# Optimization experiments

Measured on AMD Instinct MI355X. Metric: run time of the kernel, lower is better.

## Reference

```python
import jax, jax.numpy as jnp
import numpy as np

EPS = 1e-4

def _softmax_kernel(data, projection_matrix, is_query):
    # data: [..., n, d], projection_matrix: [m, d]
    d = data.shape[-1]
    m = projection_matrix.shape[0]
    data_normalizer = 1.0 / (d ** 0.25)
    ratio = 1.0 / (m ** 0.5)
    # [..., n, m]
    data_dash = jnp.einsum('...id,jd->...ij', data_normalizer * data, projection_matrix)
    # ||x||^2 / 2 * normalizer^2, shape [..., n, 1]
    diag_data = (jnp.sum(data * data, axis=-1) * 0.5 * data_normalizer ** 2)[..., None]
    if is_query:
        stab = jnp.max(data_dash, axis=-1, keepdims=True)
    else:
        stab = jnp.max(data_dash)
    return ratio * (jnp.exp(data_dash - diag_data - stab) + EPS)

def _linear_attention(q, k, v):
    # q,k: [..., n, m] feature maps; v: [..., n, e]
    D_inv = 1.0 / jnp.einsum('...nd,...d->...n', q, k.sum(axis=-2))
    context = jnp.einsum('...nd,...ne->...de', k, v)  # [..., m, e]
    return jnp.einsum('...de,...nd,...n->...ne', context, q, D_inv)

def setup_inputs() -> dict:
    key = jax.random.key(0)
    k1, k2, k3, k4 = jax.random.split(key, 4)
    B, H, N, D, M = 8, 8, 4096, 64, 266
    return {
        'q': jax.random.normal(k1, (B, H, N, D), dtype=jnp.float32),
        'k': jax.random.normal(k2, (B, H, N, D), dtype=jnp.float32),
        'v': jax.random.normal(k3, (B, H, N, D), dtype=jnp.float32),
        'projection_matrix': jax.random.normal(k4, (M, D), dtype=jnp.float32),
    }

def reference(q, k, v, projection_matrix):
    q_prime = _softmax_kernel(q, projection_matrix, is_query=True)
    k_prime = _softmax_kernel(k, projection_matrix, is_query=False)
    return _linear_attention(q_prime, k_prime, v)
```

## Files before the change

### kernel.cpp

```cpp
#include <hip/hip_runtime.h>
#include <math.h>

#define BH    64
#define NSEQ  4096
#define DDIM  64
#define MDIM  266
#define MPAD  272
#define KTS   40
#define RATIO 0.06131393394849658f
#define NORMF 0.35355339059327373f
#define DIAGF 0.0625f
#define EPSF  1e-4f

typedef __attribute__((ext_vector_type(8))) short bf16x8;
typedef __attribute__((ext_vector_type(4))) float f32x4;

__device__ __forceinline__ unsigned fenc(float f) {
  unsigned u = __float_as_uint(f);
  return (u & 0x80000000u) ? ~u : (u | 0x80000000u);
}
__device__ __forceinline__ float fdec(unsigned u) {
  return (u & 0x80000000u) ? __uint_as_float(u & 0x7fffffffu) : __uint_as_float(~u);
}

__device__ __forceinline__ void split1(float x, unsigned short& h, unsigned short& l) {
  unsigned ux = __float_as_uint(x);
  float hf = __uint_as_float(ux & 0xffff0000u);
  h = (unsigned short)(ux >> 16);
  l = (unsigned short)(__float_as_uint(x - hf) >> 16);
}

__device__ __forceinline__ void splitf(float4 a, float4 b, bf16x8& hi, bf16x8& lo) {
  float x[8] = {a.x, a.y, a.z, a.w, b.x, b.y, b.z, b.w};
#pragma unroll
  for (int e = 0; e < 8; ++e) {
    unsigned short h, l;
    split1(x[e], h, l);
    hi[e] = (short)h;
    lo[e] = (short)l;
  }
}

__device__ __forceinline__ f32x4 mfma3(bf16x8 ah, bf16x8 al, bf16x8 bh, bf16x8 bl, f32x4 acc) {
  acc = __builtin_amdgcn_mfma_f32_16x16x32_bf16(ah, bh, acc, 0, 0, 0);
  acc = __builtin_amdgcn_mfma_f32_16x16x32_bf16(ah, bl, acc, 0, 0, 0);
  acc = __builtin_amdgcn_mfma_f32_16x16x32_bf16(al, bh, acc, 0, 0, 0);
  return acc;
}

__global__ __launch_bounds__(256) void pprep_kernel(const float* __restrict__ proj,
                                                    short* __restrict__ phi,
                                                    short* __restrict__ plo) {
  int idx = blockIdx.x * 256 + threadIdx.x;
  if (idx >= MPAD * DDIM) return;
  int j = idx >> 6;
  float x = (j < MDIM) ? proj[idx] : 0.f;
  unsigned short h, l;
  split1(x, h, l);
  phi[idx] = (short)h;
  plo[idx] = (short)l;
}

__global__ __launch_bounds__(256) void kmax_kernel(const float* __restrict__ k,
                                                   const short* __restrict__ phi,
                                                   const short* __restrict__ plo,
                                                   unsigned* __restrict__ kmax) {
  __shared__ float sK[64 * 76];
  __shared__ float wmax[4];
  const int tid = threadIdx.x;
  const int lane = tid & 63, wv = tid >> 6, lrow = lane & 15, lgrp = lane >> 4;

  float tmax = -1e30f;
  for (int it = 0; it < 8; ++it) {
    const int chunk = blockIdx.x * 8 + it;
    const int bh = chunk >> 6, ch = chunk & 63;
    const float* kb = k + ((size_t)bh * NSEQ + (size_t)ch * 64) * DDIM;
    __syncthreads();
#pragma unroll
    for (int t = 0; t < 4; ++t) {
      int fid = tid + t * 256, r = fid >> 4, d4 = fid & 15;
      *(float4*)&sK[r * 76 + d4 * 4] = ((const float4*)kb)[fid];
    }
    __syncthreads();

    bf16x8 ahi[2], alo[2];
#pragma unroll
    for (int s = 0; s < 2; ++s) {
      const float* p = &sK[(wv * 16 + lrow) * 76 + s * 32 + lgrp * 8];
      splitf(*(const float4*)p, *(const float4*)(p + 4), ahi[s], alo[s]);
    }

#pragma unroll
    for (int jt = 0; jt < 17; ++jt) {
      f32x4 acc = {0.f, 0.f, 0.f, 0.f};
#pragma unroll
      for (int s = 0; s < 2; ++s) {
        const size_t bo = ((size_t)(jt * 16 + lrow)) * DDIM + s * 32 + lgrp * 8;
        acc = mfma3(ahi[s], alo[s], *(const bf16x8*)(phi + bo), *(const bf16x8*)(plo + bo), acc);
      }
      if (jt < 16 || lrow < 10) {
#pragma unroll
        for (int i = 0; i < 4; ++i) tmax = fmaxf(tmax, acc[i]);
      }
    }
  }
#pragma unroll
  for (int off = 32; off; off >>= 1) tmax = fmaxf(tmax, __shfl_xor(tmax, off));
  if (lane == 0) wmax[wv] = tmax;
  __syncthreads();
  if (tid == 0) {
    float m = fmaxf(fmaxf(wmax[0], wmax[1]), fmaxf(wmax[2], wmax[3]));
    atomicMax(kmax, fenc(m * NORMF));
  }
}

__device__ __forceinline__ float dash_reg(int jt, const bf16x8* ahi, const bf16x8* alo,
                                          const bf16x8* ph, const bf16x8* pl,
                                          const float* sDiag, float stab,
                                          unsigned short* kThi, unsigned short* kTlo,
                                          int lrow, int lgrp) {
  float kssum = 0.f;
  const int jg = jt * 16 + lrow;
#pragma unroll
  for (int m = 0; m < 2; ++m) {
    f32x4 d = {0.f, 0.f, 0.f, 0.f};
#pragma unroll
    for (int s = 0; s < 2; ++s)
      d = mfma3(ahi[m * 2 + s], alo[m * 2 + s], ph[s], pl[s], d);
    ushort4 h4, l4;
#pragma unroll
    for (int i = 0; i < 4; ++i) {
      const int nl = m * 16 + lgrp * 4 + i;
      float kd = d[i] * NORMF;
      float kp = (jg < MDIM) ? RATIO * (__expf(kd - sDiag[nl] - stab) + EPSF) : 0.f;
      kssum += kp;
      unsigned short h, l;
      split1(kp, h, l);
      ((unsigned short*)&h4)[i] = h;
      ((unsigned short*)&l4)[i] = l;
    }
    *(ushort4*)&kThi[(size_t)jg * KTS + m * 16 + lgrp * 4] = h4;
    *(ushort4*)&kTlo[(size_t)jg * KTS + m * 16 + lgrp * 4] = l4;
  }
  return kssum;
}

__global__ __launch_bounds__(256, 2) void ctx_kernel(const float* __restrict__ k,
                                                     const float* __restrict__ v,
                                                     const short* __restrict__ phi,
                                                     const short* __restrict__ plo,
                                                     const unsigned* __restrict__ kmaxp,
                                                     float* __restrict__ ctxp,
                                                     float* __restrict__ ksump) {
  __shared__ unsigned short kThi[MPAD * KTS];
  __shared__ unsigned short kTlo[MPAD * KTS];
  __shared__ float sV[32 * 68];
  __shared__ float sDiag[32];
  float* sK = (float*)kThi;

  const int tid = threadIdx.x;
  const int lane = tid & 63, wv = tid >> 6, lrow = lane & 15, lgrp = lane >> 4;
  const int bh = blockIdx.x & 63, c8 = blockIdx.x >> 6;
  const float stab = fdec(*kmaxp);
  const float* kb = k + ((size_t)bh * NSEQ + (size_t)c8 * 512) * DDIM;
  const float* vb = v + ((size_t)bh * NSEQ + (size_t)c8 * 512) * DDIM;

  bf16x8 pfh[4][2], pfl[4][2];
#pragma unroll
  for (int t = 0; t < 4; ++t)
#pragma unroll
    for (int s = 0; s < 2; ++s) {
      const size_t bo = ((size_t)((t * 4 + wv) * 16 + lrow)) * DDIM + s * 32 + lgrp * 8;
      pfh[t][s] = *(const bf16x8*)(phi + bo);
      pfl[t][s] = *(const bf16x8*)(plo + bo);
    }
  bf16x8 pfh4[2], pfl4[2];
  if (wv == 0) {
#pragma unroll
    for (int s = 0; s < 2; ++s) {
      const size_t bo = ((size_t)(256 + lrow)) * DDIM + s * 32 + lgrp * 8;
      pfh4[s] = *(const bf16x8*)(phi + bo);
      pfl4[s] = *(const bf16x8*)(plo + bo);
    }
  }

  f32x4 acc[17];
#pragma unroll
  for (int jt = 0; jt < 17; ++jt) acc[jt] = (f32x4){0.f, 0.f, 0.f, 0.f};
  float ks[5] = {0.f, 0.f, 0.f, 0.f, 0.f};

  for (int rt = 0; rt < 16; ++rt) {
#pragma unroll
    for (int t = 0; t < 2; ++t) {
      int fid = tid + t * 256, r = fid >> 4, d4 = fid & 15;
      *(float4*)&sK[r * 76 + d4 * 4] = ((const float4*)(kb + (size_t)rt * 32 * DDIM))[fid];
      *(float4*)&sV[r * 68 + d4 * 4] = ((const float4*)(vb + (size_t)rt * 32 * DDIM))[fid];
    }
    __syncthreads();
    if (tid < 32) {
      float s = 0.f;
      const float* row = &sK[tid * 76];
#pragma unroll
      for (int d = 0; d < 64; d += 4) {
        float4 x = *(const float4*)(row + d);
        s = fmaf(x.x, x.x, fmaf(x.y, x.y, fmaf(x.z, x.z, fmaf(x.w, x.w, s))));
      }
      sDiag[tid] = s * DIAGF;
    }
    bf16x8 ahi[4], alo[4];
#pragma unroll
    for (int m = 0; m < 2; ++m)
#pragma unroll
      for (int s = 0; s < 2; ++s) {
        const float* p = &sK[(m * 16 + lrow) * 76 + s * 32 + lgrp * 8];
        splitf(*(const float4*)p, *(const float4*)(p + 4), ahi[m * 2 + s], alo[m * 2 + s]);
      }
    bf16x8 vbh, vbl;
    {
      float tv[8];
#pragma unroll
      for (int q = 0; q < 8; ++q) tv[q] = sV[(lgrp * 8 + q) * 68 + wv * 16 + lrow];
      splitf(make_float4(tv[0], tv[1], tv[2], tv[3]),
             make_float4(tv[4], tv[5], tv[6], tv[7]), vbh, vbl);
    }
    __syncthreads();

#pragma unroll
    for (int t = 0; t < 4; ++t)
      ks[t] += dash_reg(t * 4 + wv, ahi, alo, pfh[t], pfl[t], sDiag, stab,
                        kThi, kTlo, lrow, lgrp);
    if (wv == 0)
      ks[4] += dash_reg(16, ahi, alo, pfh4, pfl4, sDiag, stab, kThi, kTlo, lrow, lgrp);
    __syncthreads();

#pragma unroll
    for (int jt = 0; jt < 17; ++jt) {
      bf16x8 ah = *(const bf16x8*)&kThi[(size_t)(jt * 16 + lrow) * KTS + lgrp * 8];
      bf16x8 al = *(const bf16x8*)&kTlo[(size_t)(jt * 16 + lrow) * KTS + lgrp * 8];
      acc[jt] = mfma3(ah, al, vbh, vbl, acc[jt]);
    }
    __syncthreads();
  }

  float* ksb = ksump + (size_t)(c8 * BH + bh) * MPAD;
#pragma unroll
  for (int t = 0; t < 4; ++t) {
    float s = ks[t];
    s += __shfl_xor(s, 16);
    s += __shfl_xor(s, 32);
    if (lgrp == 0) ksb[(t * 4 + wv) * 16 + lrow] = s;
  }
  if (wv == 0) {
    float s = ks[4];
    s += __shfl_xor(s, 16);
    s += __shfl_xor(s, 32);
    if (lgrp == 0) ksb[256 + lrow] = s;
  }
  float* cxb = ctxp + (size_t)(c8 * BH + bh) * MPAD * DDIM;
#pragma unroll
  for (int jt = 0; jt < 17; ++jt)
#pragma unroll
    for (int i = 0; i < 4; ++i)
      cxb[(size_t)(jt * 16 + lgrp * 4 + i) * DDIM + wv * 16 + lrow] = acc[jt][i];
}

__global__ __launch_bounds__(256) void reduce_kernel(const float* __restrict__ ctxp,
                                                     const float* __restrict__ ksump,
                                                     float* __restrict__ ctx,
                                                     float* __restrict__ ksum) {
  const size_t SL = (size_t)BH * MPAD * DDIM;
  const int gid = blockIdx.x * 256 + threadIdx.x;
  if (gid < (int)(SL / 4)) {
    float4 s = make_float4(0.f, 0.f, 0.f, 0.f);
#pragma unroll
    for (int c = 0; c < 8; ++c) {
      float4 x = ((const float4*)ctxp)[c * (SL / 4) + gid];
      s.x += x.x; s.y += x.y; s.z += x.z; s.w += x.w;
    }
    ((float4*)ctx)[gid] = s;
  }
  if (gid < BH * MPAD) {
    float s = 0.f;
#pragma unroll
    for (int c = 0; c < 8; ++c) s += ksump[(size_t)c * BH * MPAD + gid];
    ksum[gid] = s;
  }
}

__global__ __launch_bounds__(256, 2) void out_kernel(const float* __restrict__ q,
                                                     const short* __restrict__ phi,
                                                     const short* __restrict__ plo,
                                                     const float* __restrict__ ctx,
                                                     const float* __restrict__ ksum,
                                                     float* __restrict__ out) {
  __shared__ float buf[64 * 76];
  __shared__ float sCtx[64 * 68];
  __shared__ float sDiag[64];
  __shared__ float sKs[MPAD];
  unsigned short* qThi = (unsigned short*)buf;
  unsigned short* qTlo = qThi + 64 * 72;
  const int tid = threadIdx.x;
  const int lane = tid & 63, wv = tid >> 6, lrow = lane & 15, lgrp = lane >> 4;
  const int bh = blockIdx.x & 63, rc = blockIdx.x >> 6;
  const float* qb = q + ((size_t)bh * NSEQ + (size_t)rc * 64) * DDIM;

#pragma unroll
  for (int t = 0; t < 4; ++t) {
    int fid = tid + t * 256, r = fid >> 4, d4 = fid & 15;
    *(float4*)&buf[r * 76 + d4 * 4] = ((const float4*)qb)[fid];
  }
  for (int t = tid; t < MPAD; t += 256) sKs[t] = (t < MDIM) ? ksum[(size_t)bh * MPAD + t] : 0.f;
  __syncthreads();
  if (tid < 64) {
    float s = 0.f;
    const float* row = &buf[tid * 76];
#pragma unroll
    for (int d = 0; d < 64; d += 4) {
      float4 x = *(const float4*)(row + d);
      s = fmaf(x.x, x.x, fmaf(x.y, x.y, fmaf(x.z, x.z, fmaf(x.w, x.w, s))));
    }
    sDiag[tid] = s * DIAGF;
  }
  bf16x8 ahi[2], alo[2];
#pragma unroll
  for (int s = 0; s < 2; ++s) {
    const float* p = &buf[(wv * 16 + lrow) * 76 + s * 32 + lgrp * 8];
    splitf(*(const float4*)p, *(const float4*)(p + 4), ahi[s], alo[s]);
  }
  __syncthreads();

  f32x4 qd[17];
#pragma unroll
  for (int jt = 0; jt < 17; ++jt) {
    f32x4 a = {0.f, 0.f, 0.f, 0.f};
#pragma unroll
    for (int s = 0; s < 2; ++s) {
      const size_t bo = ((size_t)(jt * 16 + lrow)) * DDIM + s * 32 + lgrp * 8;
      a = mfma3(ahi[s], alo[s], *(const bf16x8*)(phi + bo), *(const bf16x8*)(plo + bo), a);
    }
#pragma unroll
    for (int i = 0; i < 4; ++i) qd[jt][i] = a[i] * NORMF;
  }

  float di[4];
#pragma unroll
  for (int i = 0; i < 4; ++i) {
    float m = -1e30f;
#pragma unroll
    for (int jt = 0; jt < 17; ++jt)
      if (jt < 16 || lrow < 10) m = fmaxf(m, qd[jt][i]);
    m = fmaxf(m, __shfl_xor(m, 1));
    m = fmaxf(m, __shfl_xor(m, 2));
    m = fmaxf(m, __shfl_xor(m, 4));
    m = fmaxf(m, __shfl_xor(m, 8));
    const float dg = sDiag[wv * 16 + lgrp * 4 + i];
    float s = 0.f;
#pragma unroll
    for (int jt = 0; jt < 17; ++jt) {
      const int jg = jt * 16 + lrow;
      float val = (jg < MDIM) ? RATIO * (__expf(qd[jt][i] - dg - m) + EPSF) : 0.f;
      qd[jt][i] = val;
      s = fmaf(val, sKs[jg], s);
    }
    s += __shfl_xor(s, 1);
    s += __shfl_xor(s, 2);
    s += __shfl_xor(s, 4);
    s += __shfl_xor(s, 8);
    di[i] = 1.0f / s;
  }

  f32x4 accO[4];
#pragma unroll
  for (int mt = 0; mt < 4; ++mt) accO[mt] = (f32x4){0.f, 0.f, 0.f, 0.f};

#pragma unroll
  for (int c = 0; c < 5; ++c) {
    const int nwr = (c < 4) ? 4 : 2;
    const int nks = (c < 4) ? 2 : 1;
    const int jn = (c < 4) ? 64 : 10;
#pragma unroll
    for (int t = 0; t < nwr; ++t) {
      const int jt = c * 4 + t;
#pragma unroll
      for (int i = 0; i < 4; ++i) {
        unsigned short h = 0, l = 0;
        if (jt < 17) split1(qd[jt][i] * di[i], h, l);
        qThi[(wv * 16 + lgrp * 4 + i) * 72 + t * 16 + lrow] = h;
        qTlo[(wv * 16 + lgrp * 4 + i) * 72 + t * 16 + lrow] = l;
      }
    }
#pragma unroll
    for (int t = 0; t < 4; ++t) {
      int fid = tid + t * 256, r = fid >> 4, e4 = fid & 15;
      if (r < jn)
        *(float4*)&sCtx[r * 68 + e4 * 4] =
            ((const float4*)(ctx + ((size_t)bh * MPAD + c * 64 + r) * DDIM))[e4];
    }
    __syncthreads();
#pragma unroll
    for (int ks2 = 0; ks2 < nks; ++ks2) {
      float tv[8];
#pragma unroll
      for (int e = 0; e < 8; ++e)
        tv[e] = sCtx[(ks2 * 32 + lgrp * 8 + e) * 68 + wv * 16 + lrow];
      bf16x8 cbh, cbl;
      splitf(make_float4(tv[0], tv[1], tv[2], tv[3]),
             make_float4(tv[4], tv[5], tv[6], tv[7]), cbh, cbl);
#pragma unroll
      for (int mt = 0; mt < 4; ++mt) {
        bf16x8 ah = *(const bf16x8*)&qThi[(mt * 16 + lrow) * 72 + ks2 * 32 + lgrp * 8];
        bf16x8 al = *(const bf16x8*)&qTlo[(mt * 16 + lrow) * 72 + ks2 * 32 + lgrp * 8];
        accO[mt] = mfma3(ah, al, cbh, cbl, accO[mt]);
      }
    }
    __syncthreads();
  }

#pragma unroll
  for (int mt = 0; mt < 4; ++mt) {
#pragma unroll
    for (int i = 0; i < 4; ++i) {
      const int r = mt * 16 + lgrp * 4 + i;
      out[((size_t)bh * NSEQ + (size_t)rc * 64 + r) * DDIM + wv * 16 + lrow] = accO[mt][i];
    }
  }
}

extern "C" void kernel_launch(void* const* d_in, const int* in_sizes, int n_in,
                              void* d_out, int out_size, void* d_ws, size_t ws_size,
                              hipStream_t stream) {
  (void)in_sizes; (void)n_in; (void)out_size; (void)ws_size;
  const float* q = (const float*)d_in[0];
  const float* k = (const float*)d_in[1];
  const float* v = (const float*)d_in[2];
  const float* proj = (const float*)d_in[3];
  float* out = (float*)d_out;

  unsigned* kmax = (unsigned*)d_ws;
  float* ctx = (float*)((char*)d_ws + 256);
  float* ksum = ctx + (size_t)BH * MPAD * DDIM;
  short* phi = (short*)(ksum + (size_t)BH * MPAD);
  short* plo = phi + (size_t)MPAD * DDIM;

  const size_t SL = (size_t)BH * MPAD * DDIM;
  float* ctxp = (float*)d_out;
  float* ksump = ctxp + 8 * SL;

  hipMemsetAsync(d_ws, 0, 256, stream);
  pprep_kernel<<<dim3((MPAD * DDIM + 255) / 256), dim3(256), 0, stream>>>(proj, phi, plo);
  kmax_kernel<<<dim3(512), dim3(256), 0, stream>>>(k, phi, plo, kmax);
  ctx_kernel<<<dim3(BH * 8), dim3(256), 0, stream>>>(k, v, phi, plo, kmax, ctxp, ksump);
  reduce_kernel<<<dim3((unsigned)(SL / 4 / 256)), dim3(256), 0, stream>>>(ctxp, ksump, ctx, ksum);
  out_kernel<<<dim3(BH * 64), dim3(256), 0, stream>>>(q, phi, plo, ctx, ksum, out);
}
```

Measured before the change: 325.2 us.

## Make out_kernel persistent per 512 rows, holding split ctx in registers

The output kernel now launches 512 blocks instead of 4096. Each block loops over 16 tiles of 32 query rows and loads the context matrix once, split into bf16 hi/lo register fragments, reusing it for every tile instead of restaging it in shared memory per 64-row block. The projection work is now divided across the four waves by feature column instead of by row. This needs cross-wave max and sum reductions through shared memory plus extra barriers per tile. Fewer blocks and heavy register use (9 hi/lo fragment pairs) may lower occupancy and latency hiding on the 256-CU device.

```diff
diff --git a/kernel.cpp b/kernel.cpp
--- a/kernel.cpp
+++ b/kernel.cpp
@@ -7,6 +7,7 @@
 #define MDIM  266
 #define MPAD  272
 #define KTS   40
+#define QTS   296
 #define RATIO 0.06131393394849658f
 #define NORMF 0.35355339059327373f
 #define DIAGF 0.0625f
@@ -293,135 +294,215 @@
                                                      const float* __restrict__ ctx,
                                                      const float* __restrict__ ksum,
                                                      float* __restrict__ out) {
-  __shared__ float buf[64 * 76];
-  __shared__ float sCtx[64 * 68];
-  __shared__ float sDiag[64];
+  __shared__ unsigned short qThi[32 * QTS];
+  __shared__ unsigned short qTlo[32 * QTS];
+  __shared__ float sQ[32 * 76];
   __shared__ float sKs[MPAD];
-  unsigned short* qThi = (unsigned short*)buf;
-  unsigned short* qTlo = qThi + 64 * 72;
+  __shared__ float sDiag[32];
+  __shared__ float sMax[4 * 32];
+  __shared__ float sSum[4 * 32];
   const int tid = threadIdx.x;
   const int lane = tid & 63, wv = tid >> 6, lrow = lane & 15, lgrp = lane >> 4;
-  const int bh = blockIdx.x & 63, rc = blockIdx.x >> 6;
-  const float* qb = q + ((size_t)bh * NSEQ + (size_t)rc * 64) * DDIM;
-
-#pragma unroll
-  for (int t = 0; t < 4; ++t) {
-    int fid = tid + t * 256, r = fid >> 4, d4 = fid & 15;
-    *(float4*)&buf[r * 76 + d4 * 4] = ((const float4*)qb)[fid];
-  }
-  for (int t = tid; t < MPAD; t += 256) sKs[t] = (t < MDIM) ? ksum[(size_t)bh * MPAD + t] : 0.f;
-  __syncthreads();
-  if (tid < 64) {
-    float s = 0.f;
-    const float* row = &buf[tid * 76];
-#pragma unroll
-    for (int d = 0; d < 64; d += 4) {
-      float4 x = *(const float4*)(row + d);
-      s = fmaf(x.x, x.x, fmaf(x.y, x.y, fmaf(x.z, x.z, fmaf(x.w, x.w, s))));
-    }
-    sDiag[tid] = s * DIAGF;
-  }
-  bf16x8 ahi[2], alo[2];
-#pragma unroll
-  for (int s = 0; s < 2; ++s) {
-    const float* p = &buf[(wv * 16 + lrow) * 76 + s * 32 + lgrp * 8];
-    splitf(*(const float4*)p, *(const float4*)(p + 4), ahi[s], alo[s]);
-  }
-  __syncthreads();
-
-  f32x4 qd[17];
-#pragma unroll
-  for (int jt = 0; jt < 17; ++jt) {
-    f32x4 a = {0.f, 0.f, 0.f, 0.f};
-#pragma unroll
-    for (int s = 0; s < 2; ++s) {
-      const size_t bo = ((size_t)(jt * 16 + lrow)) * DDIM + s * 32 + lgrp * 8;
-      a = mfma3(ahi[s], alo[s], *(const bf16x8*)(phi + bo), *(const bf16x8*)(plo + bo), a);
-    }
-#pragma unroll
-    for (int i = 0; i < 4; ++i) qd[jt][i] = a[i] * NORMF;
-  }
-
-  float di[4];
-#pragma unroll
-  for (int i = 0; i < 4; ++i) {
-    float m = -1e30f;
-#pragma unroll
-    for (int jt = 0; jt < 17; ++jt)
-      if (jt < 16 || lrow < 10) m = fmaxf(m, qd[jt][i]);
-    m = fmaxf(m, __shfl_xor(m, 1));
-    m = fmaxf(m, __shfl_xor(m, 2));
-    m = fmaxf(m, __shfl_xor(m, 4));
-    m = fmaxf(m, __shfl_xor(m, 8));
-    const float dg = sDiag[wv * 16 + lgrp * 4 + i];
-    float s = 0.f;
-#pragma unroll
-    for (int jt = 0; jt < 17; ++jt) {
-      const int jg = jt * 16 + lrow;
-      float val = (jg < MDIM) ? RATIO * (__expf(qd[jt][i] - dg - m) + EPSF) : 0.f;
-      qd[jt][i] = val;
-      s = fmaf(val, sKs[jg], s);
-    }
-    s += __shfl_xor(s, 1);
-    s += __shfl_xor(s, 2);
-    s += __shfl_xor(s, 4);
-    s += __shfl_xor(s, 8);
-    di[i] = 1.0f / s;
-  }
-
-  f32x4 accO[4];
-#pragma unroll
-  for (int mt = 0; mt < 4; ++mt) accO[mt] = (f32x4){0.f, 0.f, 0.f, 0.f};
-
-#pragma unroll
-  for (int c = 0; c < 5; ++c) {
-    const int nwr = (c < 4) ? 4 : 2;
-    const int nks = (c < 4) ? 2 : 1;
-    const int jn = (c < 4) ? 64 : 10;
-#pragma unroll
-    for (int t = 0; t < nwr; ++t) {
-      const int jt = c * 4 + t;
+  const int bh = blockIdx.x & 63, c8 = blockIdx.x >> 6;
+  const float* qb = q + ((size_t)bh * NSEQ + (size_t)c8 * 512) * DDIM;
+
+  for (int idx = tid; idx < 512; idx += 256) {
+    const int r = idx >> 4, cc = 272 + (idx & 15);
+    qThi[r * QTS + cc] = 0;
+    qTlo[r * QTS + cc] = 0;
+  }
+  for (int t = tid; t < MPAD; t += 256) sKs[t] = ksum[(size_t)bh * MPAD + t];
+
+  bf16x8 cbh[9], cbl[9];
+#pragma unroll
+  for (int kst = 0; kst < 9; ++kst) {
+    float tv[8];
+#pragma unroll
+    for (int qq = 0; qq < 8; ++qq) {
+      const int j = kst * 32 + lgrp * 8 + qq;
+      tv[qq] = (j < MPAD) ? ctx[((size_t)bh * MPAD + j) * DDIM + wv * 16 + lrow] : 0.f;
+    }
+    splitf(make_float4(tv[0], tv[1], tv[2], tv[3]),
+           make_float4(tv[4], tv[5], tv[6], tv[7]), cbh[kst], cbl[kst]);
+  }
+
+  for (int rt = 0; rt < 16; ++rt) {
+    __syncthreads();
+#pragma unroll
+    for (int t = 0; t < 2; ++t) {
+      int fid = tid + t * 256, r = fid >> 4, d4 = fid & 15;
+      *(float4*)&sQ[r * 76 + d4 * 4] = ((const float4*)(qb + (size_t)rt * 32 * DDIM))[fid];
+    }
+    __syncthreads();
+    if (tid < 32) {
+      float s = 0.f;
+      const float* row = &sQ[tid * 76];
+#pragma unroll
+      for (int d = 0; d < 64; d += 4) {
+        float4 x = *(const float4*)(row + d);
+        s = fmaf(x.x, x.x, fmaf(x.y, x.y, fmaf(x.z, x.z, fmaf(x.w, x.w, s))));
+      }
+      sDiag[tid] = s * DIAGF;
+    }
+    bf16x8 ahi[4], alo[4];
+#pragma unroll
+    for (int m = 0; m < 2; ++m)
+#pragma unroll
+      for (int s = 0; s < 2; ++s) {
+        const float* p = &sQ[(m * 16 + lrow) * 76 + s * 32 + lgrp * 8];
+        splitf(*(const float4*)p, *(const float4*)(p + 4), ahi[m * 2 + s], alo[m * 2 + s]);
+      }
+    __syncthreads();
+
+    f32x4 qd[4][2];
+    f32x4 qd4[2] = {(f32x4){0.f, 0.f, 0.f, 0.f}, (f32x4){0.f, 0.f, 0.f, 0.f}};
+#pragma unroll
+    for (int t = 0; t < 4; ++t) {
+      const int jt = t * 4 + wv;
+      const size_t bo = ((size_t)(jt * 16 + lrow)) * DDIM + lgrp * 8;
+      bf16x8 ph0 = *(const bf16x8*)(phi + bo);
+      bf16x8 pl0 = *(const bf16x8*)(plo + bo);
+      bf16x8 ph1 = *(const bf16x8*)(phi + bo + 32);
+      bf16x8 pl1 = *(const bf16x8*)(plo + bo + 32);
+#pragma unroll
+      for (int m = 0; m < 2; ++m) {
+        f32x4 d = {0.f, 0.f, 0.f, 0.f};
+        d = mfma3(ahi[m * 2 + 0], alo[m * 2 + 0], ph0, pl0, d);
+        d = mfma3(ahi[m * 2 + 1], alo[m * 2 + 1], ph1, pl1, d);
+        qd[t][m] = d * NORMF;
+      }
+    }
+    if (wv == 0) {
+      const size_t bo = ((size_t)(256 + lrow)) * DDIM + lgrp * 8;
+      bf16x8 ph0 = *(const bf16x8*)(phi + bo);
+      bf16x8 pl0 = *(const bf16x8*)(plo + bo);
+      bf16x8 ph1 = *(const bf16x8*)(phi + bo + 32);
+      bf16x8 pl1 = *(const bf16x8*)(plo + bo + 32);
+#pragma unroll
+      for (int m = 0; m < 2; ++m) {
+        f32x4 d = {0.f, 0.f, 0.f, 0.f};
+        d = mfma3(ahi[m * 2 + 0], alo[m * 2 + 0], ph0, pl0, d);
+        d = mfma3(ahi[m * 2 + 1], alo[m * 2 + 1], ph1, pl1, d);
+        qd4[m] = d * NORMF;
+      }
+    }
+
+#pragma unroll
+    for (int m = 0; m < 2; ++m)
 #pragma unroll
       for (int i = 0; i < 4; ++i) {
-        unsigned short h = 0, l = 0;
-        if (jt < 17) split1(qd[jt][i] * di[i], h, l);
-        qThi[(wv * 16 + lgrp * 4 + i) * 72 + t * 16 + lrow] = h;
-        qTlo[(wv * 16 + lgrp * 4 + i) * 72 + t * 16 + lrow] = l;
-      }
-    }
+        float mx = fmaxf(fmaxf(qd[0][m][i], qd[1][m][i]), fmaxf(qd[2][m][i], qd[3][m][i]));
+        if (wv == 0 && lrow < 10) mx = fmaxf(mx, qd4[m][i]);
+        mx = fmaxf(mx, __shfl_xor(mx, 1));
+        mx = fmaxf(mx, __shfl_xor(mx, 2));
+        mx = fmaxf(mx, __shfl_xor(mx, 4));
+        mx = fmaxf(mx, __shfl_xor(mx, 8));
+        if (lrow == 0) sMax[wv * 32 + m * 16 + lgrp * 4 + i] = mx;
+      }
+    __syncthreads();
+
+    float mrow[2][4], dgr[2][4], srow[2][4];
+#pragma unroll
+    for (int m = 0; m < 2; ++m)
+#pragma unroll
+      for (int i = 0; i < 4; ++i) {
+        const int row = m * 16 + lgrp * 4 + i;
+        mrow[m][i] = fmaxf(fmaxf(sMax[row], sMax[32 + row]),
+                           fmaxf(sMax[64 + row], sMax[96 + row]));
+        dgr[m][i] = sDiag[row];
+        srow[m][i] = 0.f;
+      }
 #pragma unroll
     for (int t = 0; t < 4; ++t) {
-      int fid = tid + t * 256, r = fid >> 4, e4 = fid & 15;
-      if (r < jn)
-        *(float4*)&sCtx[r * 68 + e4 * 4] =
-            ((const float4*)(ctx + ((size_t)bh * MPAD + c * 64 + r) * DDIM))[e4];
-    }
-    __syncthreads();
-#pragma unroll
-    for (int ks2 = 0; ks2 < nks; ++ks2) {
-      float tv[8];
-#pragma unroll
-      for (int e = 0; e < 8; ++e)
-        tv[e] = sCtx[(ks2 * 32 + lgrp * 8 + e) * 68 + wv * 16 + lrow];
-      bf16x8 cbh, cbl;
-      splitf(make_float4(tv[0], tv[1], tv[2], tv[3]),
-             make_float4(tv[4], tv[5], tv[6], tv[7]), cbh, cbl);
-#pragma unroll
-      for (int mt = 0; mt < 4; ++mt) {
-        bf16x8 ah = *(const bf16x8*)&qThi[(mt * 16 + lrow) * 72 + ks2 * 32 + lgrp * 8];
-        bf16x8 al = *(const bf16x8*)&qTlo[(mt * 16 + lrow) * 72 + ks2 * 32 + lgrp * 8];
-        accO[mt] = mfma3(ah, al, cbh, cbl, accO[mt]);
-      }
-    }
-    __syncthreads();
-  }
-
-#pragma unroll
-  for (int mt = 0; mt < 4; ++mt) {
-#pragma unroll
-    for (int i = 0; i < 4; ++i) {
-      const int r = mt * 16 + lgrp * 4 + i;
-      out[((size_t)bh * NSEQ + (size_t)rc * 64 + r) * DDIM + wv * 16 + lrow] = accO[mt][i];
+      const int jg = (t * 4 + wv) * 16 + lrow;
+      const float ksj = sKs[jg];
+#pragma unroll
+      for (int m = 0; m < 2; ++m)
+#pragma unroll
+        for (int i = 0; i < 4; ++i) {
+          float val = RATIO * (__expf(qd[t][m][i] - dgr[m][i] - mrow[m][i]) + EPSF);
+          qd[t][m][i] = val;
+          srow[m][i] = fmaf(val, ksj, srow[m][i]);
+        }
+    }
+    if (wv == 0) {
+      const int jg = 256 + lrow;
+      const float ksj = sKs[jg];
+#pragma unroll
+      for (int m = 0; m < 2; ++m)
+#pragma unroll
+        for (int i = 0; i < 4; ++i) {
+          float val = (jg < MDIM) ? RATIO * (__expf(qd4[m][i] - dgr[m][i] - mrow[m][i]) + EPSF)
+                                  : 0.f;
+          qd4[m][i] = val;
+          srow[m][i] = fmaf(val, ksj, srow[m][i]);
+        }
+    }
+#pragma unroll
+    for (int m = 0; m < 2; ++m)
+#pragma unroll
+      for (int i = 0; i < 4; ++i) {
+        float s = srow[m][i];
+        s += __shfl_xor(s, 1);
+        s += __shfl_xor(s, 2);
+        s += __shfl_xor(s, 4);
+        s += __shfl_xor(s, 8);
+        if (lrow == 0) sSum[wv * 32 + m * 16 + lgrp * 4 + i] = s;
+      }
+    __syncthreads();
+
+    float di[2][4];
+#pragma unroll
+    for (int m = 0; m < 2; ++m)
+#pragma unroll
+      for (int i = 0; i < 4; ++i) {
+        const int row = m * 16 + lgrp * 4 + i;
+        di[m][i] = 1.0f / (sSum[row] + sSum[32 + row] + sSum[64 + row] + sSum[96 + row]);
+      }
+
+#pragma unroll
+    for (int t = 0; t < 4; ++t) {
+      const int j = (t * 4 + wv) * 16 + lrow;
+#pragma unroll
+      for (int m = 0; m < 2; ++m)
+#pragma unroll
+        for (int i = 0; i < 4; ++i) {
+          unsigned short h, l;
+          split1(qd[t][m][i] * di[m][i], h, l);
+          const int n = m * 16 + lgrp * 4 + i;
+          qThi[n * QTS + j] = h;
+          qTlo[n * QTS + j] = l;
+        }
+    }
+    if (wv == 0) {
+      const int j = 256 + lrow;
+#pragma unroll
+      for (int m = 0; m < 2; ++m)
+#pragma unroll
+        for (int i = 0; i < 4; ++i) {
+          unsigned short h, l;
+          split1(qd4[m][i] * di[m][i], h, l);
+          const int n = m * 16 + lgrp * 4 + i;
+          qThi[n * QTS + j] = h;
+          qTlo[n * QTS + j] = l;
+        }
+    }
+    __syncthreads();
+
+#pragma unroll
+    for (int mt = 0; mt < 2; ++mt) {
+      f32x4 acc = {0.f, 0.f, 0.f, 0.f};
+#pragma unroll
+      for (int kst = 0; kst < 9; ++kst) {
+        bf16x8 ah = *(const bf16x8*)&qThi[(mt * 16 + lrow) * QTS + kst * 32 + lgrp * 8];
+        bf16x8 al = *(const bf16x8*)&qTlo[(mt * 16 + lrow) * QTS + kst * 32 + lgrp * 8];
+        acc = mfma3(ah, al, cbh[kst], cbl[kst], acc);
+      }
+#pragma unroll
+      for (int i = 0; i < 4; ++i) {
+        const int n = rt * 32 + mt * 16 + lgrp * 4 + i;
+        out[((size_t)bh * NSEQ + (size_t)c8 * 512 + n) * DDIM + wv * 16 + lrow] = acc[i];
+      }
     }
   }
 }
@@ -451,5 +532,5 @@
   kmax_kernel<<<dim3(512), dim3(256), 0, stream>>>(k, phi, plo, kmax);
   ctx_kernel<<<dim3(BH * 8), dim3(256), 0, stream>>>(k, v, phi, plo, kmax, ctxp, ksump);
   reduce_kernel<<<dim3((unsigned)(SL / 4 / 256)), dim3(256), 0, stream>>>(ctxp, ksump, ctx, ksum);
-  out_kernel<<<dim3(BH * 64), dim3(256), 0, stream>>>(q, phi, plo, ctx, ksum, out);
-}
+  out_kernel<<<dim3(BH * 8), dim3(256), 0, stream>>>(q, phi, plo, ctx, ksum, out);
+}
```

New measurement: 303.9 us. 6.5% less time.
